# Kernel tuning notes

Hardware: AMD Instinct MI355X
Metric: run time of the kernel (lower is better)

## Reference

```python
import jax, jax.numpy as jnp
import numpy as np

N_STEPS = 2
MAX_STEP = 1.0
EPS64 = float(np.finfo(np.float64).eps)


def _sphere_log(p, q):
    # log map on unit sphere, tangent at p pointing to q; p,q: [..., D]
    cos = jnp.clip(jnp.sum(p * q, axis=-1, keepdims=True), -1.0, 1.0)
    u = q - cos * p
    un = jnp.linalg.norm(u, axis=-1, keepdims=True)
    theta = jnp.arccos(cos)
    return theta * u / (un + 1e-12)


def _sphere_exp(p, v):
    # exp map on unit sphere; jnp.sinc(n/pi) = sin(n)/n (stable at 0)
    n = jnp.linalg.norm(v, axis=-1, keepdims=True)
    x = jnp.cos(n) * p + jnp.sinc(n / jnp.pi) * v
    return x / jnp.linalg.norm(x, axis=-1, keepdims=True)


def setup_inputs() -> dict:
    key = jax.random.key(0)
    ks = jax.random.split(key, 6)
    N, C, D, E = 50000, 16, 3, 1600000
    nodes = jax.random.normal(ks[0], (N, C, D), dtype=jnp.float32)
    nodes = nodes / jnp.linalg.norm(nodes, axis=-1, keepdims=True)  # points on S^2
    edge_w = jax.random.uniform(ks[1], (E,), dtype=jnp.float32)
    senders = jax.random.randint(ks[2], (E,), 0, N, dtype=jnp.int32)
    receivers = jax.random.randint(ks[3], (E,), 0, N, dtype=jnp.int32)
    t_sqrt = 1.0 + 0.3 * jax.random.normal(ks[4], (C,), dtype=jnp.float32)
    delta_sqrt = 1.0 + 0.3 * jax.random.normal(ks[5], (C,), dtype=jnp.float32)
    return {"nodes": nodes, "edge_w": edge_w, "t_sqrt": t_sqrt,
            "delta_sqrt": delta_sqrt, "senders": senders, "receivers": receivers}


def reference(nodes, edge_w, t_sqrt, delta_sqrt, senders, receivers):
    N = nodes.shape[0]
    t = (t_sqrt ** 2) / N_STEPS            # per-channel time, split across Euler steps
    delta = delta_sqrt ** 2                 # per-channel min step size
    deg = jax.ops.segment_sum(edge_w, senders, num_segments=N)  # [N]

    def laplace(x):
        # graph Laplacian of manifold-valued signal: weighted mean of log maps, negated
        logs = _sphere_log(x[senders], x[receivers])              # [E, C, D]
        agg = jax.ops.segment_sum(edge_w[:, None, None] * logs, senders, num_segments=N)
        return -agg / (deg[:, None, None] + 1e-12)                # [N, C, D]

    def step(x, _):
        v = laplace(x)
        nrm = jnp.sqrt(jnp.sum(v * v, axis=-1) + EPS64)           # [N, C]
        alp = jax.nn.sigmoid(nrm - delta[None, :])
        scale = jnp.where(nrm * alp <= MAX_STEP, alp, MAX_STEP / nrm)
        v = -(v * scale[..., None]) * t[None, :, None]
        return _sphere_exp(x, v), None

    x, _ = jax.lax.scan(step, nodes, None, length=N_STEPS, unroll=N_STEPS)
    return x
```

## Files before the change

kernel.cpp:

```cpp
#include <hip/hip_runtime.h>
#include <math.h>


constexpr float EPS64F = 2.2204460492503131e-16f;
constexpr float PI_F   = 3.14159265358979323846f;
constexpr int   SR_BITS = 14;
constexpr int   CH_BITS = 15;

typedef int   vi4 __attribute__((ext_vector_type(4)));
typedef float vf4 __attribute__((ext_vector_type(4)));
typedef float vf2 __attribute__((ext_vector_type(2)));


__global__ __launch_bounds__(256) void lhist_kernel(
    const int* __restrict__ snd, unsigned char* __restrict__ pos,
    int* __restrict__ partial2, int E, int NC) {
  __shared__ int h[1 << SR_BITS];
  int tid = threadIdx.x;
  int c = blockIdx.x, s = blockIdx.y;
  for (int i = tid; i < (1 << SR_BITS); i += 256) h[i] = 0;
  __syncthreads();
  int base = c << CH_BITS;
  int cnt = min(1 << CH_BITS, E - base);
  int s0 = s << SR_BITS;
  const vi4* snd4 = (const vi4*)(snd + base);
  int cnt4 = cnt >> 2;
  for (int i = tid; i < cnt4; i += 256) {
    vi4 sv = snd4[i];
    int e = base + (i << 2);
    int v;
    v = sv.x - s0; if ((unsigned)v < (1u << SR_BITS)) pos[e]     = (unsigned char)atomicAdd(&h[v], 1);
    v = sv.y - s0; if ((unsigned)v < (1u << SR_BITS)) pos[e + 1] = (unsigned char)atomicAdd(&h[v], 1);
    v = sv.z - s0; if ((unsigned)v < (1u << SR_BITS)) pos[e + 2] = (unsigned char)atomicAdd(&h[v], 1);
    v = sv.w - s0; if ((unsigned)v < (1u << SR_BITS)) pos[e + 3] = (unsigned char)atomicAdd(&h[v], 1);
  }
  if (tid == 0) {
    for (int i = cnt4 << 2; i < cnt; ++i) {
      int v = snd[base + i] - s0;
      if ((unsigned)v < (1u << SR_BITS))
        pos[base + i] = (unsigned char)atomicAdd(&h[v], 1);
    }
  }
  __syncthreads();
  int* dst = partial2 + ((size_t)(s * NC + c) << SR_BITS);
  for (int i = tid; i < (1 << SR_BITS); i += 256) dst[i] = h[i];
}

__global__ __launch_bounds__(256) void scan1_kernel(
    const int* __restrict__ partial2, int* __restrict__ boff,
    int* __restrict__ tot, int N, int NC) {
  int v = blockIdx.x * 256 + threadIdx.x;
  if (v >= N) return;
  int s = v >> SR_BITS, lv = v & ((1 << SR_BITS) - 1);
  int run = 0;
  for (int c = 0; c < NC; ++c) {
    int t = partial2[((size_t)(s * NC + c) << SR_BITS) + lv];
    boff[(size_t)c * N + v] = run;
    run += t;
  }
  tot[v] = run;
}

__global__ __launch_bounds__(1024) void scanA_kernel(
    const int* __restrict__ tot, int* __restrict__ row_start,
    int* __restrict__ btot, int N) {
  __shared__ int wsum[16];
  int tid = threadIdx.x;
  int lane = tid & 63, wave = tid >> 6;
  int i = blockIdx.x * 1024 + tid;
  int v = (i < N) ? tot[i] : 0;
  int incl = v;
  #pragma unroll
  for (int off = 1; off < 64; off <<= 1) {
    int t = __shfl_up(incl, off, 64);
    if (lane >= off) incl += t;
  }
  if (lane == 63) wsum[wave] = incl;
  __syncthreads();
  if (wave == 0 && lane < 16) {
    int wincl = wsum[lane];
    #pragma unroll
    for (int off = 1; off < 16; off <<= 1) {
      int t = __shfl_up(wincl, off, 64);
      if (lane >= off) wincl += t;
    }
    wsum[lane] = wincl;
  }
  __syncthreads();
  int woff = (wave > 0) ? wsum[wave - 1] : 0;
  if (i < N) row_start[i] = woff + incl - v;
  if (tid == 0) btot[blockIdx.x] = wsum[15];
}

__global__ __launch_bounds__(64) void scanB_kernel(
    const int* __restrict__ btot, int* __restrict__ boffb,
    int* __restrict__ row_start, int nb, int N) {
  int lane = threadIdx.x;
  int v = (lane < nb) ? btot[lane] : 0;
  int incl = v;
  #pragma unroll
  for (int off = 1; off < 64; off <<= 1) {
    int t = __shfl_up(incl, off, 64);
    if (lane >= off) incl += t;
  }
  if (lane < nb) boffb[lane] = incl - v;
  if (lane == 63) row_start[N] = incl;
}

__global__ __launch_bounds__(1024) void scanC_kernel(
    int* __restrict__ row_start, const int* __restrict__ boffb, int N) {
  int i = blockIdx.x * 1024 + threadIdx.x;
  if (i < N) row_start[i] += boffb[blockIdx.x];
}

__global__ __launch_bounds__(256) void scanD_kernel(
    int* __restrict__ boff, const int* __restrict__ row_start, int N, int NC) {
  int v = blockIdx.x * 256 + threadIdx.x;
  if (v >= N) return;
  int rs = row_start[v];
  for (int c = 0; c < NC; ++c) boff[(size_t)c * N + v] += rs;
}

__global__ __launch_bounds__(256) void fill_kernel(
    const vi4* __restrict__ snd4, const vi4* __restrict__ rcv4,
    const vf4* __restrict__ ew4, const unsigned char* __restrict__ pos,
    const int* __restrict__ boff, long long* __restrict__ pair,
    const int* __restrict__ snd, const int* __restrict__ rcv,
    const float* __restrict__ ew, int N, int E) {
  int tid = threadIdx.x;
  int E4 = E >> 2;
  #pragma unroll
  for (int gg = 0; gg < 2; ++gg) {
    int g = blockIdx.x * 512 + gg * 256 + tid;
    if (g < E4) {
      int e = g << 2;
      const int* bc = boff + (size_t)(e >> CH_BITS) * N;
      vi4 s = __builtin_nontemporal_load(&snd4[g]);
      vi4 r = __builtin_nontemporal_load(&rcv4[g]);
      vf4 w = __builtin_nontemporal_load(&ew4[g]);
      unsigned pb = *(const unsigned*)(pos + e);
      pair[bc[s.x] + (pb & 255u)] =
          (long long)(((unsigned long long)(unsigned)__float_as_int(w.x) << 32) | (unsigned)(r.x * 48));
      pair[bc[s.y] + ((pb >> 8) & 255u)] =
          (long long)(((unsigned long long)(unsigned)__float_as_int(w.y) << 32) | (unsigned)(r.y * 48));
      pair[bc[s.z] + ((pb >> 16) & 255u)] =
          (long long)(((unsigned long long)(unsigned)__float_as_int(w.z) << 32) | (unsigned)(r.z * 48));
      pair[bc[s.w] + (pb >> 24)] =
          (long long)(((unsigned long long)(unsigned)__float_as_int(w.w) << 32) | (unsigned)(r.w * 48));
    }
  }
  if (blockIdx.x == 0 && tid == 0) {
    for (int e = E4 << 2; e < E; ++e) {
      pair[boff[(size_t)(e >> CH_BITS) * N + snd[e]] + pos[e]] =
          (long long)(((unsigned long long)(unsigned)__float_as_int(ew[e]) << 32) | (unsigned)(rcv[e] * 48));
    }
    for (int z = 0; z < 16; ++z) pair[(size_t)E + z] = 0;
  }
}


__device__ __forceinline__ void edge_accum_pk(
    vf2 p0, vf2 p1, vf2 p2, vf2 q0, vf2 q1, vf2 q2, vf2 w,
    vf2& a0, vf2& a1, vf2& a2) {
  vf2 cs = p0 * q0 + p1 * q1 + p2 * q2;
  cs = __builtin_elementwise_min(vf2{1.f, 1.f},
       __builtin_elementwise_max(vf2{-1.f, -1.f}, cs));
  vf2 u0 = q0 - cs * p0;
  vf2 u1 = q1 - cs * p1;
  vf2 u2 = q2 - cs * p2;
  vf2 un2 = __builtin_elementwise_max(u0 * u0 + u1 * u1 + u2 * u2,
                                      vf2{1e-24f, 1e-24f});
  vf2 ax = __builtin_elementwise_abs(cs);
  vf2 s = __builtin_elementwise_sqrt(vf2{1.f, 1.f} - ax);
  vf2 poly = ((ax * -0.0187293f + 0.0742610f) * ax - 0.2121144f) * ax
             + 1.5707288f;
  vf2 th = s * poly;
  vf2 theta;
  theta.x = (cs.x >= 0.0f) ? th.x : (PI_F - th.x);
  theta.y = (cs.y >= 0.0f) ? th.y : (PI_F - th.y);
  vf2 rsq;
  rsq.x = __builtin_amdgcn_rsqf(un2.x);
  rsq.y = __builtin_amdgcn_rsqf(un2.y);
  vf2 coef = w * theta * rsq;
  a0 += coef * u0;
  a1 += coef * u1;
  a2 += coef * u2;
}

__device__ __forceinline__ void node_step(
    float a0, float a1, float a2, float ws, float p0, float p1, float p2,
    float ts, float dsv, float& y0, float& y1, float& y2) {
  float invdg = __builtin_amdgcn_rcpf(ws + 1e-12f);
  float g0 = a0 * invdg, g1 = a1 * invdg, g2 = a2 * invdg;
  float nrm = sqrtf(fmaf(g0, g0, fmaf(g1, g1, g2 * g2)) + EPS64F);
  float tch = ts * ts * 0.5f;
  float dch = dsv * dsv;
  float alp = __builtin_amdgcn_rcpf(1.0f + __expf(dch - nrm));
  float scale = (nrm * alp <= 1.0f) ? alp : __builtin_amdgcn_rcpf(nrm);
  float f = scale * tch;
  float v0 = g0 * f, v1 = g1 * f, v2 = g2 * f;
  float nv = sqrtf(fmaf(v0, v0, fmaf(v1, v1, v2 * v2)));
  float cn = __cosf(nv);
  float sc = (nv > 1e-20f) ? (__sinf(nv) * __builtin_amdgcn_rcpf(nv)) : 1.0f;
  float t0 = fmaf(cn, p0, sc * v0);
  float t1 = fmaf(cn, p1, sc * v1);
  float t2 = fmaf(cn, p2, sc * v2);
  float inv = __builtin_amdgcn_rsqf(fmaf(t0, t0, fmaf(t1, t1, t2 * t2)));
  y0 = t0 * inv; y1 = t1 * inv; y2 = t2 * inv;
}

__global__ __launch_bounds__(256) void flowp_kernel(
    const float* __restrict__ xin, const int* __restrict__ row_start,
    const long long* __restrict__ pair, const float* __restrict__ tsq,
    const float* __restrict__ dsq, float* __restrict__ xout, int N) {
  int node = blockIdx.x * 4 + (threadIdx.x >> 6);
  if (node >= N) return;
  int lane = threadIdx.x & 63;
  int c = lane & 15;
  int k = lane >> 4;
  int c3 = c * 3;
  int beg = row_start[node];
  int end = row_start[node + 1];
  int ip = node * 48 + c3;
  float ps0 = xin[ip], ps1 = xin[ip + 1], ps2 = xin[ip + 2];
  vf2 p0 = {ps0, ps0}, p1 = {ps1, ps1}, p2 = {ps2, ps2};
  vf2 a0 = {0.f, 0.f}, a1 = {0.f, 0.f}, a2 = {0.f, 0.f}, wsv = {0.f, 0.f};
  int iters = (end - beg + 15) >> 4;
  int j = beg + k;
  for (int t = 0; t < iters; ++t, j += 16) {
    long long e0 = __builtin_nontemporal_load(&pair[j]);
    long long e1 = __builtin_nontemporal_load(&pair[j + 4]);
    long long e2 = __builtin_nontemporal_load(&pair[j + 8]);
    long long e3 = __builtin_nontemporal_load(&pair[j + 12]);
    float w0 = (j      < end) ? __int_as_float((int)(e0 >> 32)) : 0.f;
    float w1 = (j + 4  < end) ? __int_as_float((int)(e1 >> 32)) : 0.f;
    float w2 = (j + 8  < end) ? __int_as_float((int)(e2 >> 32)) : 0.f;
    float w3 = (j + 12 < end) ? __int_as_float((int)(e3 >> 32)) : 0.f;
    const float* q0p = xin + ((int)e0 + c3);
    const float* q1p = xin + ((int)e1 + c3);
    const float* q2p = xin + ((int)e2 + c3);
    const float* q3p = xin + ((int)e3 + c3);
    float qa0 = q0p[0], qa1 = q0p[1], qa2 = q0p[2];
    float qb0 = q1p[0], qb1 = q1p[1], qb2 = q1p[2];
    float qc0 = q2p[0], qc1 = q2p[1], qc2 = q2p[2];
    float qd0 = q3p[0], qd1 = q3p[1], qd2 = q3p[2];
    vf2 wA = {w0, w1}, wB = {w2, w3};
    edge_accum_pk(p0, p1, p2, vf2{qa0, qb0}, vf2{qa1, qb1}, vf2{qa2, qb2},
                  wA, a0, a1, a2);
    edge_accum_pk(p0, p1, p2, vf2{qc0, qd0}, vf2{qc1, qd1}, vf2{qc2, qd2},
                  wB, a0, a1, a2);
    wsv += wA + wB;
  }
  float A0 = a0.x + a0.y, A1 = a1.x + a1.y, A2 = a2.x + a2.y;
  float ws = wsv.x + wsv.y;
  A0 += __shfl_xor(A0, 16); A1 += __shfl_xor(A1, 16);
  A2 += __shfl_xor(A2, 16); ws += __shfl_xor(ws, 16);
  A0 += __shfl_xor(A0, 32); A1 += __shfl_xor(A1, 32);
  A2 += __shfl_xor(A2, 32); ws += __shfl_xor(ws, 32);
  if (k == 0) {
    float y0, y1, y2;
    node_step(A0, A1, A2, ws, ps0, ps1, ps2, tsq[c], dsq[c], y0, y1, y2);
    xout[ip] = y0; xout[ip + 1] = y1; xout[ip + 2] = y2;
  }
}

static inline size_t al16(size_t x) { return (x + 15) & ~(size_t)15; }

extern "C" void kernel_launch(void* const* d_in, const int* in_sizes, int n_in,
                              void* d_out, int out_size, void* d_ws, size_t ws_size,
                              hipStream_t stream) {
  const float* nodes = (const float*)d_in[0];
  const float* ew    = (const float*)d_in[1];
  const float* tsq   = (const float*)d_in[2];
  const float* dsq   = (const float*)d_in[3];
  const int*   snd   = (const int*)d_in[4];
  const int*   rcv   = (const int*)d_in[5];
  float* out = (float*)d_out;

  int E = in_sizes[1];
  int N = in_sizes[0] / 48;

  int NS = (N + (1 << SR_BITS) - 1) >> SR_BITS;
  int NC = (E + (1 << CH_BITS) - 1) >> CH_BITS;

  size_t rsB   = al16((size_t)(N + 4) * 4);
  size_t auxB  = 512;
  size_t pairB = al16((size_t)(E + 16) * 8);
  size_t p2B   = al16(((size_t)NS * NC << SR_BITS) * 4);
  size_t boffB = al16((size_t)NC * N * 4);
  size_t totB  = al16((size_t)N * 4);

  char* base = (char*)d_ws;
  int*           row_start = (int*)base;
  int*           btot      = (int*)(base + rsB);
  int*           boffb     = btot + 64;
  long long*     pair      = (long long*)(base + rsB + auxB);
  int*           partial2  = (int*)(base + rsB + auxB + pairB);
  int*           boff      = (int*)(base + rsB + auxB + pairB + p2B);
  int*           tot       = (int*)(base + rsB + auxB + pairB + p2B + boffB);
  unsigned char* pos       = (unsigned char*)(base + rsB + auxB + pairB + p2B + boffB + totB);
  float*         xtmp      = (float*)partial2;

  int E4  = E >> 2;
  int nb  = (N + 1023) / 1024;
  int nb2 = (N + 255) / 256;
  int fbk = (E4 + 511) / 512;
  int nfb = (N + 3) / 4;

  lhist_kernel<<<dim3(NC, NS), 256, 0, stream>>>(snd, pos, partial2, E, NC);
  scan1_kernel<<<nb2, 256, 0, stream>>>(partial2, boff, tot, N, NC);
  scanA_kernel<<<nb, 1024, 0, stream>>>(tot, row_start, btot, N);
  scanB_kernel<<<1, 64, 0, stream>>>(btot, boffb, row_start, nb, N);
  scanC_kernel<<<nb, 1024, 0, stream>>>(row_start, boffb, N);
  scanD_kernel<<<nb2, 256, 0, stream>>>(boff, row_start, N, NC);
  fill_kernel<<<fbk, 256, 0, stream>>>((const vi4*)snd, (const vi4*)rcv,
                                       (const vf4*)ew, pos, boff, pair,
                                       snd, rcv, ew, N, E);

  flowp_kernel<<<nfb, 256, 0, stream>>>(nodes, row_start, pair, tsq, dsq, xtmp, N);
  flowp_kernel<<<nfb, 256, 0, stream>>>(xtmp, row_start, pair, tsq, dsq, out, N);
}
```

Before: 298.4 us.

## Pad node states to float4 and split channels into four groups per node

Node states are converted to a padded float4-per-channel layout, so each receiver gather becomes one 16-byte vector load instead of three scalar loads, and the stored receiver offset changes to index*16. The flow kernel now launches four blocks per node group, each handling 4 channels with 16 edge lanes per channel. This improves gather coalescing but re-reads the pair array four times per step and adds a conversion kernel plus extra workspace. The final step writes back to the unpadded 48-float output.

```diff
diff --git a/kernel.cpp b/kernel.cpp
--- a/kernel.cpp
+++ b/kernel.cpp
@@ -140,22 +140,31 @@
       vf4 w = __builtin_nontemporal_load(&ew4[g]);
       unsigned pb = *(const unsigned*)(pos + e);
       pair[bc[s.x] + (pb & 255u)] =
-          (long long)(((unsigned long long)(unsigned)__float_as_int(w.x) << 32) | (unsigned)(r.x * 48));
+          (long long)(((unsigned long long)(unsigned)__float_as_int(w.x) << 32) | (unsigned)(r.x * 16));
       pair[bc[s.y] + ((pb >> 8) & 255u)] =
-          (long long)(((unsigned long long)(unsigned)__float_as_int(w.y) << 32) | (unsigned)(r.y * 48));
+          (long long)(((unsigned long long)(unsigned)__float_as_int(w.y) << 32) | (unsigned)(r.y * 16));
       pair[bc[s.z] + ((pb >> 16) & 255u)] =
-          (long long)(((unsigned long long)(unsigned)__float_as_int(w.z) << 32) | (unsigned)(r.z * 48));
+          (long long)(((unsigned long long)(unsigned)__float_as_int(w.z) << 32) | (unsigned)(r.z * 16));
       pair[bc[s.w] + (pb >> 24)] =
-          (long long)(((unsigned long long)(unsigned)__float_as_int(w.w) << 32) | (unsigned)(r.w * 48));
+          (long long)(((unsigned long long)(unsigned)__float_as_int(w.w) << 32) | (unsigned)(r.w * 16));
     }
   }
   if (blockIdx.x == 0 && tid == 0) {
     for (int e = E4 << 2; e < E; ++e) {
       pair[boff[(size_t)(e >> CH_BITS) * N + snd[e]] + pos[e]] =
-          (long long)(((unsigned long long)(unsigned)__float_as_int(ew[e]) << 32) | (unsigned)(rcv[e] * 48));
-    }
-    for (int z = 0; z < 16; ++z) pair[(size_t)E + z] = 0;
-  }
+          (long long)(((unsigned long long)(unsigned)__float_as_int(ew[e]) << 32) | (unsigned)(rcv[e] * 16));
+    }
+    for (int z = 0; z < 32; ++z) pair[(size_t)E + z] = 0;
+  }
+}
+
+__global__ __launch_bounds__(256) void conv_kernel(
+    const float* __restrict__ xf, vf4* __restrict__ xp, int NC16) {
+  int t = blockIdx.x * 256 + threadIdx.x;
+  if (t >= NC16) return;
+  vf4 v;
+  v.x = xf[t * 3]; v.y = xf[t * 3 + 1]; v.z = xf[t * 3 + 2]; v.w = 0.f;
+  xp[t] = v;
 }
 
 
@@ -209,58 +218,57 @@
   y0 = t0 * inv; y1 = t1 * inv; y2 = t2 * inv;
 }
 
-__global__ __launch_bounds__(256) void flowp_kernel(
-    const float* __restrict__ xin, const int* __restrict__ row_start,
+__global__ __launch_bounds__(256) void flowx_kernel(
+    const vf4* __restrict__ xp, const int* __restrict__ row_start,
     const long long* __restrict__ pair, const float* __restrict__ tsq,
-    const float* __restrict__ dsq, float* __restrict__ xout, int N) {
-  int node = blockIdx.x * 4 + (threadIdx.x >> 6);
+    const float* __restrict__ dsq, vf4* __restrict__ yp,
+    float* __restrict__ out48, int N) {
+  int b = blockIdx.x;
+  int g = b & 3;
+  int node = (b >> 2) * 4 + (threadIdx.x >> 6);
   if (node >= N) return;
   int lane = threadIdx.x & 63;
-  int c = lane & 15;
-  int k = lane >> 4;
-  int c3 = c * 3;
+  int c = g * 4 + (lane & 3);
+  int k = lane >> 2;
   int beg = row_start[node];
   int end = row_start[node + 1];
-  int ip = node * 48 + c3;
-  float ps0 = xin[ip], ps1 = xin[ip + 1], ps2 = xin[ip + 2];
-  vf2 p0 = {ps0, ps0}, p1 = {ps1, ps1}, p2 = {ps2, ps2};
+  vf4 p = xp[node * 16 + c];
+  vf2 p0 = {p.x, p.x}, p1 = {p.y, p.y}, p2 = {p.z, p.z};
   vf2 a0 = {0.f, 0.f}, a1 = {0.f, 0.f}, a2 = {0.f, 0.f}, wsv = {0.f, 0.f};
-  int iters = (end - beg + 15) >> 4;
+  int iters = (end - beg + 31) >> 5;
   int j = beg + k;
-  for (int t = 0; t < iters; ++t, j += 16) {
+  for (int t = 0; t < iters; ++t, j += 32) {
     long long e0 = __builtin_nontemporal_load(&pair[j]);
-    long long e1 = __builtin_nontemporal_load(&pair[j + 4]);
-    long long e2 = __builtin_nontemporal_load(&pair[j + 8]);
-    long long e3 = __builtin_nontemporal_load(&pair[j + 12]);
+    long long e1 = __builtin_nontemporal_load(&pair[j + 16]);
     float w0 = (j      < end) ? __int_as_float((int)(e0 >> 32)) : 0.f;
-    float w1 = (j + 4  < end) ? __int_as_float((int)(e1 >> 32)) : 0.f;
-    float w2 = (j + 8  < end) ? __int_as_float((int)(e2 >> 32)) : 0.f;
-    float w3 = (j + 12 < end) ? __int_as_float((int)(e3 >> 32)) : 0.f;
-    const float* q0p = xin + ((int)e0 + c3);
-    const float* q1p = xin + ((int)e1 + c3);
-    const float* q2p = xin + ((int)e2 + c3);
-    const float* q3p = xin + ((int)e3 + c3);
-    float qa0 = q0p[0], qa1 = q0p[1], qa2 = q0p[2];
-    float qb0 = q1p[0], qb1 = q1p[1], qb2 = q1p[2];
-    float qc0 = q2p[0], qc1 = q2p[1], qc2 = q2p[2];
-    float qd0 = q3p[0], qd1 = q3p[1], qd2 = q3p[2];
-    vf2 wA = {w0, w1}, wB = {w2, w3};
-    edge_accum_pk(p0, p1, p2, vf2{qa0, qb0}, vf2{qa1, qb1}, vf2{qa2, qb2},
-                  wA, a0, a1, a2);
-    edge_accum_pk(p0, p1, p2, vf2{qc0, qd0}, vf2{qc1, qd1}, vf2{qc2, qd2},
-                  wB, a0, a1, a2);
-    wsv += wA + wB;
+    float w1 = (j + 16 < end) ? __int_as_float((int)(e1 >> 32)) : 0.f;
+    vf4 qa = xp[(int)e0 + c];
+    vf4 qb = xp[(int)e1 + c];
+    vf2 w = {w0, w1};
+    edge_accum_pk(p0, p1, p2, vf2{qa.x, qb.x}, vf2{qa.y, qb.y},
+                  vf2{qa.z, qb.z}, w, a0, a1, a2);
+    wsv += w;
   }
   float A0 = a0.x + a0.y, A1 = a1.x + a1.y, A2 = a2.x + a2.y;
   float ws = wsv.x + wsv.y;
+  A0 += __shfl_xor(A0, 4);  A1 += __shfl_xor(A1, 4);
+  A2 += __shfl_xor(A2, 4);  ws += __shfl_xor(ws, 4);
+  A0 += __shfl_xor(A0, 8);  A1 += __shfl_xor(A1, 8);
+  A2 += __shfl_xor(A2, 8);  ws += __shfl_xor(ws, 8);
   A0 += __shfl_xor(A0, 16); A1 += __shfl_xor(A1, 16);
   A2 += __shfl_xor(A2, 16); ws += __shfl_xor(ws, 16);
   A0 += __shfl_xor(A0, 32); A1 += __shfl_xor(A1, 32);
   A2 += __shfl_xor(A2, 32); ws += __shfl_xor(ws, 32);
   if (k == 0) {
     float y0, y1, y2;
-    node_step(A0, A1, A2, ws, ps0, ps1, ps2, tsq[c], dsq[c], y0, y1, y2);
-    xout[ip] = y0; xout[ip + 1] = y1; xout[ip + 2] = y2;
+    node_step(A0, A1, A2, ws, p.x, p.y, p.z, tsq[c], dsq[c], y0, y1, y2);
+    if (out48) {
+      int ip = node * 48 + c * 3;
+      out48[ip] = y0; out48[ip + 1] = y1; out48[ip + 2] = y2;
+    } else {
+      vf4 v; v.x = y0; v.y = y1; v.z = y2; v.w = 0.f;
+      yp[node * 16 + c] = v;
+    }
   }
 }
 
@@ -285,10 +293,11 @@
 
   size_t rsB   = al16((size_t)(N + 4) * 4);
   size_t auxB  = 512;
-  size_t pairB = al16((size_t)(E + 16) * 8);
+  size_t pairB = al16((size_t)(E + 32) * 8);
   size_t p2B   = al16(((size_t)NS * NC << SR_BITS) * 4);
   size_t boffB = al16((size_t)NC * N * 4);
   size_t totB  = al16((size_t)N * 4);
+  size_t posB  = al16((size_t)E);
 
   char* base = (char*)d_ws;
   int*           row_start = (int*)base;
@@ -299,14 +308,17 @@
   int*           boff      = (int*)(base + rsB + auxB + pairB + p2B);
   int*           tot       = (int*)(base + rsB + auxB + pairB + p2B + boffB);
   unsigned char* pos       = (unsigned char*)(base + rsB + auxB + pairB + p2B + boffB + totB);
-  float*         xtmp      = (float*)partial2;
+  vf4*           xp0       = (vf4*)(base + rsB + auxB + pairB + p2B + boffB + totB + posB);
+  vf4*           xtmp      = (vf4*)partial2;
 
   int E4  = E >> 2;
   int nb  = (N + 1023) / 1024;
   int nb2 = (N + 255) / 256;
   int fbk = (E4 + 511) / 512;
-  int nfb = (N + 3) / 4;
-
+  int cb  = (N * 16 + 255) / 256;
+  int gb  = ((N + 3) / 4) * 4;
+
+  conv_kernel<<<cb, 256, 0, stream>>>(nodes, xp0, N * 16);
   lhist_kernel<<<dim3(NC, NS), 256, 0, stream>>>(snd, pos, partial2, E, NC);
   scan1_kernel<<<nb2, 256, 0, stream>>>(partial2, boff, tot, N, NC);
   scanA_kernel<<<nb, 1024, 0, stream>>>(tot, row_start, btot, N);
@@ -317,6 +329,8 @@
                                        (const vf4*)ew, pos, boff, pair,
                                        snd, rcv, ew, N, E);
 
-  flowp_kernel<<<nfb, 256, 0, stream>>>(nodes, row_start, pair, tsq, dsq, xtmp, N);
-  flowp_kernel<<<nfb, 256, 0, stream>>>(xtmp, row_start, pair, tsq, dsq, out, N);
-}
+  flowx_kernel<<<gb, 256, 0, stream>>>(xp0, row_start, pair, tsq, dsq,
+                                       xtmp, (float*)0, N);
+  flowx_kernel<<<gb, 256, 0, stream>>>(xtmp, row_start, pair, tsq, dsq,
+                                       (vf4*)0, out, N);
+}
```

Result: slower. 498.4 us (+67.0%).

## Gather neighbor points as padded fp16 with fp32 fallback for near-parallel edges

Applied to the files above, without the earlier changes.

Adds a copy of the node positions in half precision, padded to 8-byte vec4 entries, so each neighbour gather in the flow kernel is one 8-byte load instead of three scalar fp32 loads. Edges whose tangent norm is small, where fp16 error would matter, are recomputed from the fp32 positions. The second step's fp16 copy is written by the first step, and the two scan fix-up kernels are merged into one launch. This adds a conversion kernel, a rare divergent reload path, and some accuracy risk from half-precision inputs to the dot product.

```diff
diff --git a/kernel.cpp b/kernel.cpp
--- a/kernel.cpp
+++ b/kernel.cpp
@@ -7,9 +7,10 @@
 constexpr int   SR_BITS = 14;
 constexpr int   CH_BITS = 15;
 
-typedef int   vi4 __attribute__((ext_vector_type(4)));
-typedef float vf4 __attribute__((ext_vector_type(4)));
-typedef float vf2 __attribute__((ext_vector_type(2)));
+typedef int      vi4 __attribute__((ext_vector_type(4)));
+typedef float    vf4 __attribute__((ext_vector_type(4)));
+typedef float    vf2 __attribute__((ext_vector_type(2)));
+typedef _Float16 vh4 __attribute__((ext_vector_type(4)));
 
 
 __global__ __launch_bounds__(256) void lhist_kernel(
@@ -107,18 +108,14 @@
   if (lane == 63) row_start[N] = incl;
 }
 
-__global__ __launch_bounds__(1024) void scanC_kernel(
-    int* __restrict__ row_start, const int* __restrict__ boffb, int N) {
-  int i = blockIdx.x * 1024 + threadIdx.x;
-  if (i < N) row_start[i] += boffb[blockIdx.x];
-}
-
-__global__ __launch_bounds__(256) void scanD_kernel(
-    int* __restrict__ boff, const int* __restrict__ row_start, int N, int NC) {
-  int v = blockIdx.x * 256 + threadIdx.x;
-  if (v >= N) return;
-  int rs = row_start[v];
-  for (int c = 0; c < NC; ++c) boff[(size_t)c * N + v] += rs;
+__global__ __launch_bounds__(256) void scanCD_kernel(
+    int* __restrict__ row_start, const int* __restrict__ boffb,
+    int* __restrict__ boff, int N, int NC) {
+  int i = blockIdx.x * 256 + threadIdx.x;
+  if (i >= N) return;
+  int rs = row_start[i] + boffb[i >> 10];
+  row_start[i] = rs;
+  for (int c = 0; c < NC; ++c) boff[(size_t)c * N + i] += rs;
 }
 
 __global__ __launch_bounds__(256) void fill_kernel(
@@ -140,27 +137,61 @@
       vf4 w = __builtin_nontemporal_load(&ew4[g]);
       unsigned pb = *(const unsigned*)(pos + e);
       pair[bc[s.x] + (pb & 255u)] =
-          (long long)(((unsigned long long)(unsigned)__float_as_int(w.x) << 32) | (unsigned)(r.x * 48));
+          (long long)(((unsigned long long)(unsigned)__float_as_int(w.x) << 32) | (unsigned)(r.x * 64));
       pair[bc[s.y] + ((pb >> 8) & 255u)] =
-          (long long)(((unsigned long long)(unsigned)__float_as_int(w.y) << 32) | (unsigned)(r.y * 48));
+          (long long)(((unsigned long long)(unsigned)__float_as_int(w.y) << 32) | (unsigned)(r.y * 64));
       pair[bc[s.z] + ((pb >> 16) & 255u)] =
-          (long long)(((unsigned long long)(unsigned)__float_as_int(w.z) << 32) | (unsigned)(r.z * 48));
+          (long long)(((unsigned long long)(unsigned)__float_as_int(w.z) << 32) | (unsigned)(r.z * 64));
       pair[bc[s.w] + (pb >> 24)] =
-          (long long)(((unsigned long long)(unsigned)__float_as_int(w.w) << 32) | (unsigned)(r.w * 48));
+          (long long)(((unsigned long long)(unsigned)__float_as_int(w.w) << 32) | (unsigned)(r.w * 64));
     }
   }
   if (blockIdx.x == 0 && tid == 0) {
     for (int e = E4 << 2; e < E; ++e) {
       pair[boff[(size_t)(e >> CH_BITS) * N + snd[e]] + pos[e]] =
-          (long long)(((unsigned long long)(unsigned)__float_as_int(ew[e]) << 32) | (unsigned)(rcv[e] * 48));
-    }
-    for (int z = 0; z < 16; ++z) pair[(size_t)E + z] = 0;
-  }
-}
-
-
-__device__ __forceinline__ void edge_accum_pk(
+          (long long)(((unsigned long long)(unsigned)__float_as_int(ew[e]) << 32) | (unsigned)(rcv[e] * 64));
+    }
+    for (int z = 0; z < 32; ++z) pair[(size_t)E + z] = 0;
+  }
+}
+
+__global__ __launch_bounds__(256) void conv_kernel(
+    const float* __restrict__ xf, _Float16* __restrict__ xh, int NC16) {
+  int t = blockIdx.x * 256 + threadIdx.x;
+  if (t >= NC16) return;
+  vh4 h;
+  h.x = (_Float16)xf[t * 3];
+  h.y = (_Float16)xf[t * 3 + 1];
+  h.z = (_Float16)xf[t * 3 + 2];
+  h.w = (_Float16)0.f;
+  *(vh4*)(xh + (size_t)t * 4) = h;
+}
+
+
+__device__ __forceinline__ void redo32(
+    const float* __restrict__ xf, int v64, int c3,
+    float P0, float P1, float P2, float w,
+    float& d0, float& d1, float& d2) {
+  const float* q = xf + ((v64 >> 6) * 48 + c3);
+  float q0 = q[0], q1 = q[1], q2 = q[2];
+  float cs = fminf(1.0f, fmaxf(-1.0f, fmaf(P0, q0, fmaf(P1, q1, P2 * q2))));
+  float u0 = fmaf(-cs, P0, q0);
+  float u1 = fmaf(-cs, P1, q1);
+  float u2 = fmaf(-cs, P2, q2);
+  float un2 = fmaxf(fmaf(u0, u0, fmaf(u1, u1, u2 * u2)), 1e-24f);
+  float ax = fabsf(cs);
+  float s = sqrtf(1.0f - ax);
+  float poly = fmaf(ax, fmaf(ax, fmaf(ax, -0.0187293f, 0.0742610f),
+                             -0.2121144f), 1.5707288f);
+  float th = s * poly;
+  float theta = (cs >= 0.0f) ? th : (PI_F - th);
+  float coef = w * theta * __builtin_amdgcn_rsqf(un2);
+  d0 = coef * u0; d1 = coef * u1; d2 = coef * u2;
+}
+
+__device__ __forceinline__ void edge_accum_pk_g(
     vf2 p0, vf2 p1, vf2 p2, vf2 q0, vf2 q1, vf2 q2, vf2 w,
+    int vA, int vB, int c3, const float* __restrict__ xf,
     vf2& a0, vf2& a1, vf2& a2) {
   vf2 cs = p0 * q0 + p1 * q1 + p2 * q2;
   cs = __builtin_elementwise_min(vf2{1.f, 1.f},
@@ -168,8 +199,8 @@
   vf2 u0 = q0 - cs * p0;
   vf2 u1 = q1 - cs * p1;
   vf2 u2 = q2 - cs * p2;
-  vf2 un2 = __builtin_elementwise_max(u0 * u0 + u1 * u1 + u2 * u2,
-                                      vf2{1e-24f, 1e-24f});
+  vf2 un2raw = u0 * u0 + u1 * u1 + u2 * u2;
+  vf2 un2 = __builtin_elementwise_max(un2raw, vf2{1e-24f, 1e-24f});
   vf2 ax = __builtin_elementwise_abs(cs);
   vf2 s = __builtin_elementwise_sqrt(vf2{1.f, 1.f} - ax);
   vf2 poly = ((ax * -0.0187293f + 0.0742610f) * ax - 0.2121144f) * ax
@@ -182,9 +213,23 @@
   rsq.x = __builtin_amdgcn_rsqf(un2.x);
   rsq.y = __builtin_amdgcn_rsqf(un2.y);
   vf2 coef = w * theta * rsq;
+  bool bx = (un2raw.x < 1e-4f) && (w.x > 0.f);
+  bool by = (un2raw.y < 1e-4f) && (w.y > 0.f);
+  if (bx) coef.x = 0.f;
+  if (by) coef.y = 0.f;
   a0 += coef * u0;
   a1 += coef * u1;
   a2 += coef * u2;
+  if (__builtin_expect(bx, 0)) {
+    float d0, d1, d2;
+    redo32(xf, vA, c3, p0.x, p1.x, p2.x, w.x, d0, d1, d2);
+    a0.x += d0; a1.x += d1; a2.x += d2;
+  }
+  if (__builtin_expect(by, 0)) {
+    float d0, d1, d2;
+    redo32(xf, vB, c3, p0.x, p1.x, p2.x, w.y, d0, d1, d2);
+    a0.y += d0; a1.y += d1; a2.y += d2;
+  }
 }
 
 __device__ __forceinline__ void node_step(
@@ -209,20 +254,21 @@
   y0 = t0 * inv; y1 = t1 * inv; y2 = t2 * inv;
 }
 
-__global__ __launch_bounds__(256) void flowp_kernel(
-    const float* __restrict__ xin, const int* __restrict__ row_start,
-    const long long* __restrict__ pair, const float* __restrict__ tsq,
-    const float* __restrict__ dsq, float* __restrict__ xout, int N) {
+__global__ __launch_bounds__(256) void flowh_kernel(
+    const _Float16* __restrict__ xh, const float* __restrict__ xf,
+    const int* __restrict__ row_start, const long long* __restrict__ pair,
+    const float* __restrict__ tsq, const float* __restrict__ dsq,
+    float* __restrict__ yf, _Float16* __restrict__ yh, int N) {
   int node = blockIdx.x * 4 + (threadIdx.x >> 6);
   if (node >= N) return;
   int lane = threadIdx.x & 63;
   int c = lane & 15;
   int k = lane >> 4;
-  int c3 = c * 3;
+  int c3 = c * 3, c4 = c * 4;
   int beg = row_start[node];
   int end = row_start[node + 1];
   int ip = node * 48 + c3;
-  float ps0 = xin[ip], ps1 = xin[ip + 1], ps2 = xin[ip + 2];
+  float ps0 = xf[ip], ps1 = xf[ip + 1], ps2 = xf[ip + 2];
   vf2 p0 = {ps0, ps0}, p1 = {ps1, ps1}, p2 = {ps2, ps2};
   vf2 a0 = {0.f, 0.f}, a1 = {0.f, 0.f}, a2 = {0.f, 0.f}, wsv = {0.f, 0.f};
   int iters = (end - beg + 15) >> 4;
@@ -236,19 +282,22 @@
     float w1 = (j + 4  < end) ? __int_as_float((int)(e1 >> 32)) : 0.f;
     float w2 = (j + 8  < end) ? __int_as_float((int)(e2 >> 32)) : 0.f;
     float w3 = (j + 12 < end) ? __int_as_float((int)(e3 >> 32)) : 0.f;
-    const float* q0p = xin + ((int)e0 + c3);
-    const float* q1p = xin + ((int)e1 + c3);
-    const float* q2p = xin + ((int)e2 + c3);
-    const float* q3p = xin + ((int)e3 + c3);
-    float qa0 = q0p[0], qa1 = q0p[1], qa2 = q0p[2];
-    float qb0 = q1p[0], qb1 = q1p[1], qb2 = q1p[2];
-    float qc0 = q2p[0], qc1 = q2p[1], qc2 = q2p[2];
-    float qd0 = q3p[0], qd1 = q3p[1], qd2 = q3p[2];
+    int v0 = (int)e0, v1 = (int)e1, v2 = (int)e2, v3 = (int)e3;
+    vh4 ha = *(const vh4*)(xh + v0 + c4);
+    vh4 hb = *(const vh4*)(xh + v1 + c4);
+    vh4 hc = *(const vh4*)(xh + v2 + c4);
+    vh4 hd = *(const vh4*)(xh + v3 + c4);
     vf2 wA = {w0, w1}, wB = {w2, w3};
-    edge_accum_pk(p0, p1, p2, vf2{qa0, qb0}, vf2{qa1, qb1}, vf2{qa2, qb2},
-                  wA, a0, a1, a2);
-    edge_accum_pk(p0, p1, p2, vf2{qc0, qd0}, vf2{qc1, qd1}, vf2{qc2, qd2},
-                  wB, a0, a1, a2);
+    edge_accum_pk_g(p0, p1, p2,
+                    vf2{(float)ha.x, (float)hb.x},
+                    vf2{(float)ha.y, (float)hb.y},
+                    vf2{(float)ha.z, (float)hb.z},
+                    wA, v0, v1, c3, xf, a0, a1, a2);
+    edge_accum_pk_g(p0, p1, p2,
+                    vf2{(float)hc.x, (float)hd.x},
+                    vf2{(float)hc.y, (float)hd.y},
+                    vf2{(float)hc.z, (float)hd.z},
+                    wB, v2, v3, c3, xf, a0, a1, a2);
     wsv += wA + wB;
   }
   float A0 = a0.x + a0.y, A1 = a1.x + a1.y, A2 = a2.x + a2.y;
@@ -260,7 +309,13 @@
   if (k == 0) {
     float y0, y1, y2;
     node_step(A0, A1, A2, ws, ps0, ps1, ps2, tsq[c], dsq[c], y0, y1, y2);
-    xout[ip] = y0; xout[ip + 1] = y1; xout[ip + 2] = y2;
+    yf[ip] = y0; yf[ip + 1] = y1; yf[ip + 2] = y2;
+    if (yh) {
+      vh4 h;
+      h.x = (_Float16)y0; h.y = (_Float16)y1; h.z = (_Float16)y2;
+      h.w = (_Float16)0.f;
+      *(vh4*)(yh + (size_t)(node * 16 + c) * 4) = h;
+    }
   }
 }
 
@@ -285,10 +340,11 @@
 
   size_t rsB   = al16((size_t)(N + 4) * 4);
   size_t auxB  = 512;
-  size_t pairB = al16((size_t)(E + 16) * 8);
+  size_t pairB = al16((size_t)(E + 32) * 8);
   size_t p2B   = al16(((size_t)NS * NC << SR_BITS) * 4);
   size_t boffB = al16((size_t)NC * N * 4);
   size_t totB  = al16((size_t)N * 4);
+  size_t posB  = al16((size_t)E);
 
   char* base = (char*)d_ws;
   int*           row_start = (int*)base;
@@ -299,24 +355,29 @@
   int*           boff      = (int*)(base + rsB + auxB + pairB + p2B);
   int*           tot       = (int*)(base + rsB + auxB + pairB + p2B + boffB);
   unsigned char* pos       = (unsigned char*)(base + rsB + auxB + pairB + p2B + boffB + totB);
+  _Float16*      xh0       = (_Float16*)(base + rsB + auxB + pairB + p2B + boffB + totB + posB);
   float*         xtmp      = (float*)partial2;
+  _Float16*      xh1       = (_Float16*)boff;
 
   int E4  = E >> 2;
   int nb  = (N + 1023) / 1024;
   int nb2 = (N + 255) / 256;
   int fbk = (E4 + 511) / 512;
+  int cb  = (N * 16 + 255) / 256;
   int nfb = (N + 3) / 4;
 
+  conv_kernel<<<cb, 256, 0, stream>>>(nodes, xh0, N * 16);
   lhist_kernel<<<dim3(NC, NS), 256, 0, stream>>>(snd, pos, partial2, E, NC);
   scan1_kernel<<<nb2, 256, 0, stream>>>(partial2, boff, tot, N, NC);
   scanA_kernel<<<nb, 1024, 0, stream>>>(tot, row_start, btot, N);
   scanB_kernel<<<1, 64, 0, stream>>>(btot, boffb, row_start, nb, N);
-  scanC_kernel<<<nb, 1024, 0, stream>>>(row_start, boffb, N);
-  scanD_kernel<<<nb2, 256, 0, stream>>>(boff, row_start, N, NC);
+  scanCD_kernel<<<nb2, 256, 0, stream>>>(row_start, boffb, boff, N, NC);
   fill_kernel<<<fbk, 256, 0, stream>>>((const vi4*)snd, (const vi4*)rcv,
                                        (const vf4*)ew, pos, boff, pair,
                                        snd, rcv, ew, N, E);
 
-  flowp_kernel<<<nfb, 256, 0, stream>>>(nodes, row_start, pair, tsq, dsq, xtmp, N);
-  flowp_kernel<<<nfb, 256, 0, stream>>>(xtmp, row_start, pair, tsq, dsq, out, N);
-}
+  flowh_kernel<<<nfb, 256, 0, stream>>>(xh0, nodes, row_start, pair,
+                                        tsq, dsq, xtmp, xh1, N);
+  flowh_kernel<<<nfb, 256, 0, stream>>>(xh1, xtmp, row_start, pair,
+                                        tsq, dsq, out, (_Float16*)0, N);
+}
```

Result: slower. 306.3 us (+2.6%).
